# Kernel tuning notes

Hardware: AMD Instinct MI355X
Metric: run time of the kernel (lower is better)

## Reference

```python
import jax, jax.numpy as jnp
import numpy as np

DIM_Q = 512
DIM_K = 512
D_Q4 = float(DIM_Q) ** 0.25  # torch: dim_q ** (1/4)
D_K4 = float(DIM_K) ** 0.25


def setup_inputs() -> dict:
    key = jax.random.key(0)
    ks = jax.random.split(key, 9)
    B, N, D_IN = 8, 4096, 512
    s_in = 1.0 / np.sqrt(D_IN)
    return {
        "x_q": jax.random.normal(ks[0], (B, N, D_IN), jnp.float32),
        "x_k": jax.random.normal(ks[1], (B, N, D_IN), jnp.float32),
        "x_v": jax.random.normal(ks[2], (B, N, D_IN), jnp.float32),
        # Linear params stored as [in, out] for x @ W + b
        "W_q": jax.random.uniform(ks[3], (D_IN, DIM_Q), jnp.float32, -s_in, s_in),
        "b_q": jax.random.uniform(ks[4], (DIM_Q,), jnp.float32, -s_in, s_in),
        "W_k": jax.random.uniform(ks[5], (D_IN, DIM_K), jnp.float32, -s_in, s_in),
        "b_k": jax.random.uniform(ks[6], (DIM_K,), jnp.float32, -s_in, s_in),
        "W_v": jax.random.uniform(ks[7], (D_IN, DIM_K), jnp.float32, -s_in, s_in),
        "b_v": jax.random.uniform(ks[8], (DIM_K,), jnp.float32, -s_in, s_in),
    }


def reference(x_q, x_k, x_v, W_q, b_q, W_k, b_k, W_v, b_v):
    Q = x_q @ W_q + b_q          # [B, n, dq]
    K = x_k @ W_k + b_k          # [B, n, dk]
    V = x_v @ W_v + b_v          # [B, n, dk]
    # softmax_row: over sequence axis (dim=-2) of Q
    A = jax.nn.softmax(Q / D_Q4, axis=-2)          # [B, n, dq]
    # softmax_col on K^T (dim=-1) == softmax over sequence axis of K
    Ks = jax.nn.softmax(K / D_K4, axis=-2)         # [B, n, dk]
    Bm = jnp.einsum("bnd,bne->bde", Ks, V)        # [B, dk, dk]
    Z = jnp.einsum("bnd,bde->bne", A, Bm)         # [B, n, dk]
    return Z
```

## Files before the change

kernel.cpp:

```cpp
#include <hip/hip_runtime.h>
#include <hip/hip_bf16.h>


typedef __bf16 bf16_t;
typedef __attribute__((ext_vector_type(8))) __bf16 bf16x8;
typedef __attribute__((ext_vector_type(4))) float f32x4;

#define MFMA_BF16 __builtin_amdgcn_mfma_f32_16x16x32_bf16

__device__ inline void async_ld16(const void* g, void* l) {
  __builtin_amdgcn_global_load_lds(
      (const __attribute__((address_space(1))) void*)g,
      (__attribute__((address_space(3))) void*)l, 16, 0, 0);
}

#define INV_D4 0.2102241038134287f

__global__ __launch_bounds__(256) void wt_kernel(
    const float* __restrict__ Wq, const float* __restrict__ Wk,
    const float* __restrict__ Wv, bf16_t* __restrict__ Wt) {
  const int z = blockIdx.z;
  const float* W = (z == 0) ? Wq : (z == 1) ? Wk : Wv;
  bf16_t* O = Wt + (size_t)z * 262144;
  __shared__ __align__(16) bf16_t tile[64 * 72];
  const int t = threadIdx.x;
  const int r = t >> 2;
  const int c4 = (t & 3) * 16;
  const int in0 = blockIdx.x * 64, out0 = blockIdx.y * 64;
  const float* src = W + (size_t)(in0 + r) * 512 + out0 + c4;
#pragma unroll
  for (int i = 0; i < 4; ++i) {
    float4 f = ((const float4*)src)[i];
    tile[(c4 + i * 4 + 0) * 72 + r] = (__bf16)f.x;
    tile[(c4 + i * 4 + 1) * 72 + r] = (__bf16)f.y;
    tile[(c4 + i * 4 + 2) * 72 + r] = (__bf16)f.z;
    tile[(c4 + i * 4 + 3) * 72 + r] = (__bf16)f.w;
  }
  __syncthreads();
  bf16x8* dst = (bf16x8*)(O + (size_t)(out0 + r) * 512 + in0 + c4);
  const bf16x8* s = (const bf16x8*)(tile + r * 72 + c4);
  dst[0] = s[0];
  dst[1] = s[1];
}

__global__ __launch_bounds__(256, 2) void proj_kernel(
    const float* __restrict__ xq, const float* __restrict__ xk,
    const float* __restrict__ xv, const bf16_t* __restrict__ Wt,
    const float* __restrict__ bq, const float* __restrict__ bk,
    const float* __restrict__ bv, bf16_t* __restrict__ Eq,
    bf16_t* __restrict__ Ft, bf16_t* __restrict__ Vt,
    float* __restrict__ Sq, float* __restrict__ Sk) {
  const int z = blockIdx.z;
  const float* X = (z == 0) ? xq : (z == 1) ? xk : xv;
  const float* bias = (z == 0) ? bq : (z == 1) ? bk : bv;
  const bf16_t* W = Wt + (size_t)z * 262144;

  __shared__ __align__(16) union U {
    struct {
      bf16_t As[4096];
      bf16_t Bs[4096];
    } s;
    bf16_t T[128 * 136];
  } u;

  const int t = threadIdx.x;
  const int lane = t & 63, w = t >> 6;
  const int quad = lane >> 4, l15 = lane & 15;
  const int m0 = blockIdx.x * 128;
  const int n0 = blockIdx.y * 128;
  const int m_off = (w & 1) * 64, n_off = (w >> 1) * 64;

  f32x4 acc[4][4];
  const f32x4 zero4 = {0.f, 0.f, 0.f, 0.f};
#pragma unroll
  for (int i = 0; i < 4; ++i)
#pragma unroll
    for (int j = 0; j < 4; ++j) acc[i][j] = zero4;

  const int ar = t >> 1;
  const int ac = (t & 1) * 16;
  const float* abase = X + (size_t)(m0 + ar) * 512 + ac;

  float4 f0 = ((const float4*)abase)[0];
  float4 f1 = ((const float4*)abase)[1];
  float4 f2 = ((const float4*)abase)[2];
  float4 f3 = ((const float4*)abase)[3];

  for (int ks = 0; ks < 16; ++ks) {
    bf16x8 p0, p1;
    p0[0] = (__bf16)f0.x; p0[1] = (__bf16)f0.y; p0[2] = (__bf16)f0.z; p0[3] = (__bf16)f0.w;
    p0[4] = (__bf16)f1.x; p0[5] = (__bf16)f1.y; p0[6] = (__bf16)f1.z; p0[7] = (__bf16)f1.w;
    p1[0] = (__bf16)f2.x; p1[1] = (__bf16)f2.y; p1[2] = (__bf16)f2.z; p1[3] = (__bf16)f2.w;
    p1[4] = (__bf16)f3.x; p1[5] = (__bf16)f3.y; p1[6] = (__bf16)f3.z; p1[7] = (__bf16)f3.w;
    ((bf16x8*)u.s.As)[(ac >> 3) * 128 + ar] = p0;
    ((bf16x8*)u.s.As)[((ac >> 3) + 1) * 128 + ar] = p1;

#pragma unroll
    for (int i = 0; i < 2; ++i) {
      const int j = w * 2 + i;
      const int k8 = j >> 1;
      const int r = ((j & 1) << 6) + lane;
      async_ld16(W + (size_t)(n0 + r) * 512 + ks * 32 + k8 * 8, u.s.Bs + j * 512);
    }
    __syncthreads();

    bf16x8 af[4], bfr[4];
#pragma unroll
    for (int mi = 0; mi < 4; ++mi)
      af[mi] = ((const bf16x8*)u.s.As)[quad * 128 + m_off + mi * 16 + l15];
#pragma unroll
    for (int ni = 0; ni < 4; ++ni)
      bfr[ni] = ((const bf16x8*)u.s.Bs)[quad * 128 + n_off + ni * 16 + l15];

    if (ks < 15) {
      const float4* p = (const float4*)(abase + (ks + 1) * 32);
      f0 = p[0]; f1 = p[1]; f2 = p[2]; f3 = p[3];
    }

#pragma unroll
    for (int mi = 0; mi < 4; ++mi)
#pragma unroll
      for (int ni = 0; ni < 4; ++ni)
        acc[mi][ni] = MFMA_BF16(af[mi], bfr[ni], acc[mi][ni], 0, 0, 0);
    __syncthreads();
  }

  const int b = m0 >> 12;
  if (z == 0) {
    float cs[4] = {0.f, 0.f, 0.f, 0.f};
#pragma unroll
    for (int ni = 0; ni < 4; ++ni) {
      const int col = n0 + n_off + ni * 16 + l15;
      const float bv_ = bias[col];
#pragma unroll
      for (int mi = 0; mi < 4; ++mi)
#pragma unroll
        for (int r = 0; r < 4; ++r) {
          const int row = m0 + m_off + mi * 16 + quad * 4 + r;
          float v = __expf((acc[mi][ni][r] + bv_) * INV_D4);
          Eq[(size_t)row * 512 + col] = (bf16_t)v;
          cs[ni] += v;
        }
    }
#pragma unroll
    for (int ni = 0; ni < 4; ++ni) {
      cs[ni] += __shfl_xor(cs[ni], 16);
      cs[ni] += __shfl_xor(cs[ni], 32);
    }
    if (lane < 16) {
#pragma unroll
      for (int ni = 0; ni < 4; ++ni)
        atomicAdd(&Sq[b * 512 + n0 + n_off + ni * 16 + lane], cs[ni]);
    }
  } else {
    const bool expm = (z == 1);
    float cs[4] = {0.f, 0.f, 0.f, 0.f};
#pragma unroll
    for (int ni = 0; ni < 4; ++ni) {
      const int colc = n_off + ni * 16 + l15;
      const float bv_ = bias[n0 + colc];
#pragma unroll
      for (int mi = 0; mi < 4; ++mi)
#pragma unroll
        for (int r = 0; r < 4; ++r) {
          const int rowr = m_off + mi * 16 + quad * 4 + r;
          float v = acc[mi][ni][r] + bv_;
          if (expm) {
            v = __expf(v * INV_D4);
            cs[ni] += v;
          }
          u.T[colc * 136 + rowr] = (bf16_t)v;
        }
    }
    if (expm) {
#pragma unroll
      for (int ni = 0; ni < 4; ++ni) {
        cs[ni] += __shfl_xor(cs[ni], 16);
        cs[ni] += __shfl_xor(cs[ni], 32);
      }
      if (lane < 16) {
#pragma unroll
        for (int ni = 0; ni < 4; ++ni)
          atomicAdd(&Sk[b * 512 + n0 + n_off + ni * 16 + lane], cs[ni]);
      }
    }
    __syncthreads();
    bf16_t* Out = expm ? Ft : Vt;
    const int nloc = m0 & 4095;
    const int c = t >> 1;
    const int rh = (t & 1) * 64;
    bf16_t* dst = Out + (size_t)b * 2097152 + (size_t)(n0 + c) * 4096 + nloc + rh;
    const bf16_t* srcT = u.T + c * 136 + rh;
#pragma unroll
    for (int j = 0; j < 8; ++j) ((bf16x8*)dst)[j] = ((const bf16x8*)srcT)[j];
  }
}

__global__ __launch_bounds__(256, 2) void bm_gemm(
    const bf16_t* __restrict__ Ft, const bf16_t* __restrict__ Vt,
    float* __restrict__ Bmp) {
  const int b = blockIdx.z >> 1;
  const int s = blockIdx.z & 1;
  const int d0 = blockIdx.x * 128;
  const int e0 = blockIdx.y * 128;
  const bf16_t* A = Ft + (size_t)b * 2097152;
  const bf16_t* B = Vt + (size_t)b * 2097152;
  float* out = Bmp + ((size_t)s * 8 + b) * 262144;

  __shared__ __align__(16) bf16_t As[4096];
  __shared__ __align__(16) bf16_t Bs[4096];

  const int t = threadIdx.x;
  const int lane = t & 63, w = t >> 6;
  const int quad = lane >> 4, l15 = lane & 15;
  const int m_off = (w & 1) * 64, n_off = (w >> 1) * 64;

  f32x4 acc[4][4];
  const f32x4 zero4 = {0.f, 0.f, 0.f, 0.f};
#pragma unroll
  for (int i = 0; i < 4; ++i)
#pragma unroll
    for (int j = 0; j < 4; ++j) acc[i][j] = zero4;

  for (int ks = 0; ks < 64; ++ks) {
    const int k0 = s * 2048 + ks * 32;
#pragma unroll
    for (int i = 0; i < 2; ++i) {
      const int j = w * 2 + i;
      const int k8 = j >> 1;
      const int r = ((j & 1) << 6) + lane;
      async_ld16(A + (size_t)(d0 + r) * 4096 + k0 + k8 * 8, As + j * 512);
      async_ld16(B + (size_t)(e0 + r) * 4096 + k0 + k8 * 8, Bs + j * 512);
    }
    __syncthreads();
    bf16x8 af[4], bfr[4];
#pragma unroll
    for (int mi = 0; mi < 4; ++mi)
      af[mi] = ((const bf16x8*)As)[quad * 128 + m_off + mi * 16 + l15];
#pragma unroll
    for (int ni = 0; ni < 4; ++ni)
      bfr[ni] = ((const bf16x8*)Bs)[quad * 128 + n_off + ni * 16 + l15];
#pragma unroll
    for (int mi = 0; mi < 4; ++mi)
#pragma unroll
      for (int ni = 0; ni < 4; ++ni)
        acc[mi][ni] = MFMA_BF16(af[mi], bfr[ni], acc[mi][ni], 0, 0, 0);
    __syncthreads();
  }

#pragma unroll
  for (int mi = 0; mi < 4; ++mi)
#pragma unroll
    for (int ni = 0; ni < 4; ++ni) {
      const int ecol = e0 + n_off + ni * 16 + l15;
#pragma unroll
      for (int r = 0; r < 4; ++r) {
        const int drow = d0 + m_off + mi * 16 + quad * 4 + r;
        out[(size_t)drow * 512 + ecol] = acc[mi][ni][r];
      }
    }
}

__global__ __launch_bounds__(256) void scale_kernel(
    const float* __restrict__ Bmp, const float* __restrict__ Sq,
    const float* __restrict__ Sk, bf16_t* __restrict__ Ct) {
  const int b = blockIdx.z;
  const int d0 = blockIdx.x * 64, e0 = blockIdx.y * 64;
  __shared__ __align__(16) bf16_t tile[64 * 72];
  const int t = threadIdx.x;
  const int r = t >> 2;
  const int c4 = (t & 3) * 16;
  const int d = d0 + r;
  const float f = 1.0f / (Sq[b * 512 + d] * Sk[b * 512 + d]);
  const float* p0 = Bmp + (size_t)b * 262144 + (size_t)d * 512 + e0 + c4;
  const float* p1 = p0 + 2097152;
#pragma unroll
  for (int i = 0; i < 4; ++i) {
    float4 v0 = ((const float4*)p0)[i];
    float4 v1 = ((const float4*)p1)[i];
    tile[(c4 + i * 4 + 0) * 72 + r] = (__bf16)((v0.x + v1.x) * f);
    tile[(c4 + i * 4 + 1) * 72 + r] = (__bf16)((v0.y + v1.y) * f);
    tile[(c4 + i * 4 + 2) * 72 + r] = (__bf16)((v0.z + v1.z) * f);
    tile[(c4 + i * 4 + 3) * 72 + r] = (__bf16)((v0.w + v1.w) * f);
  }
  __syncthreads();
  bf16x8* dst = (bf16x8*)(Ct + (size_t)b * 262144 + (size_t)(e0 + r) * 512 + d0 + c4);
  const bf16x8* s = (const bf16x8*)(tile + r * 72 + c4);
  dst[0] = s[0];
  dst[1] = s[1];
}

__global__ __launch_bounds__(256, 2) void z_gemm(
    const bf16_t* __restrict__ Eq, const bf16_t* __restrict__ Ct,
    float* __restrict__ out) {
  __shared__ __align__(16) bf16_t As[4096];
  __shared__ __align__(16) bf16_t Bs[4096];

  const int t = threadIdx.x;
  const int lane = t & 63, w = t >> 6;
  const int quad = lane >> 4, l15 = lane & 15;
  const int m0 = blockIdx.x * 128;
  const int n0 = blockIdx.y * 128;
  const int batch = m0 >> 12;
  const bf16_t* Bt = Ct + (size_t)batch * 262144;
  const int m_off = (w & 1) * 64, n_off = (w >> 1) * 64;

  f32x4 acc[4][4];
  const f32x4 zero4 = {0.f, 0.f, 0.f, 0.f};
#pragma unroll
  for (int i = 0; i < 4; ++i)
#pragma unroll
    for (int j = 0; j < 4; ++j) acc[i][j] = zero4;

  for (int ks = 0; ks < 16; ++ks) {
    const int k0 = ks * 32;
#pragma unroll
    for (int i = 0; i < 2; ++i) {
      const int j = w * 2 + i;
      const int k8 = j >> 1;
      const int r = ((j & 1) << 6) + lane;
      async_ld16(Eq + (size_t)(m0 + r) * 512 + k0 + k8 * 8, As + j * 512);
      async_ld16(Bt + (size_t)(n0 + r) * 512 + k0 + k8 * 8, Bs + j * 512);
    }
    __syncthreads();
    bf16x8 af[4], bfr[4];
#pragma unroll
    for (int mi = 0; mi < 4; ++mi)
      af[mi] = ((const bf16x8*)As)[quad * 128 + m_off + mi * 16 + l15];
#pragma unroll
    for (int ni = 0; ni < 4; ++ni)
      bfr[ni] = ((const bf16x8*)Bs)[quad * 128 + n_off + ni * 16 + l15];
#pragma unroll
    for (int mi = 0; mi < 4; ++mi)
#pragma unroll
      for (int ni = 0; ni < 4; ++ni)
        acc[mi][ni] = MFMA_BF16(af[mi], bfr[ni], acc[mi][ni], 0, 0, 0);
    __syncthreads();
  }

#pragma unroll
  for (int mi = 0; mi < 4; ++mi)
#pragma unroll
    for (int ni = 0; ni < 4; ++ni) {
      const int col = n0 + n_off + ni * 16 + l15;
#pragma unroll
      for (int r = 0; r < 4; ++r) {
        const int row = m0 + m_off + mi * 16 + quad * 4 + r;
        out[(size_t)row * 512 + col] = acc[mi][ni][r];
      }
    }
}

extern "C" void kernel_launch(void* const* d_in, const int* in_sizes, int n_in,
                              void* d_out, int out_size, void* d_ws,
                              size_t ws_size, hipStream_t stream) {
  const float* xq = (const float*)d_in[0];
  const float* xk = (const float*)d_in[1];
  const float* xv = (const float*)d_in[2];
  const float* Wq = (const float*)d_in[3];
  const float* bq = (const float*)d_in[4];
  const float* Wk = (const float*)d_in[5];
  const float* bk = (const float*)d_in[6];
  const float* Wv = (const float*)d_in[7];
  const float* bv = (const float*)d_in[8];
  float* out = (float*)d_out;

  char* ws = (char*)d_ws;
  bf16_t* Eq = (bf16_t*)(ws + 0);
  bf16_t* Ft = (bf16_t*)(ws + 33554432);
  bf16_t* Vt = (bf16_t*)(ws + 67108864);
  bf16_t* Wt = (bf16_t*)(ws + 100663296);
  float* Sq = (float*)(ws + 102236160);
  float* Sk = (float*)(ws + 102252544);
  float* Bmp = (float*)(ws + 102268928);
  bf16_t* Ct = (bf16_t*)(ws + 33554432);

  hipMemsetAsync(ws + 102236160, 0, 32768, stream);

  wt_kernel<<<dim3(8, 8, 3), 256, 0, stream>>>(Wq, Wk, Wv, Wt);
  proj_kernel<<<dim3(256, 4, 3), 256, 0, stream>>>(xq, xk, xv, Wt, bq, bk, bv,
                                                   Eq, Ft, Vt, Sq, Sk);
  bm_gemm<<<dim3(4, 4, 16), 256, 0, stream>>>(Ft, Vt, Bmp);
  scale_kernel<<<dim3(8, 8, 8), 256, 0, stream>>>(Bmp, Sq, Sk, Ct);
  z_gemm<<<dim3(256, 4, 1), 256, 0, stream>>>(Eq, Ct, out);
}
```

Before: 439.3 us.

## Pre-convert inputs to bf16 and compute K/V projections transposed directly

Adds a separate fp32-to-bf16 conversion pass that stages the inputs in the output buffer, so the projection GEMM can load both operands with async global-to-LDS copies. For K and V the GEMM is swapped to produce the transposed result directly, removing the LDS transpose stage. The K column sums move into a separate reduction kernel instead of atomics. This adds extra global traffic (writing and re-reading the bf16 copies, plus the reduction pass), extra launches, and output stores that are only partly coalesced.

```diff
diff --git a/kernel.cpp b/kernel.cpp
--- a/kernel.cpp
+++ b/kernel.cpp
@@ -43,32 +43,43 @@
   dst[1] = s[1];
 }
 
+__global__ __launch_bounds__(256) void conv_kernel(
+    const float* __restrict__ a, const float* __restrict__ b,
+    bf16_t* __restrict__ oa, bf16_t* __restrict__ ob) {
+  const float* src = (blockIdx.z == 0) ? a : b;
+  bf16_t* dst = (blockIdx.z == 0) ? oa : ob;
+  const size_t i = ((size_t)blockIdx.x * 256 + threadIdx.x) * 8;
+  float4 f0 = ((const float4*)(src + i))[0];
+  float4 f1 = ((const float4*)(src + i))[1];
+  bf16x8 p;
+  p[0] = (__bf16)f0.x; p[1] = (__bf16)f0.y; p[2] = (__bf16)f0.z; p[3] = (__bf16)f0.w;
+  p[4] = (__bf16)f1.x; p[5] = (__bf16)f1.y; p[6] = (__bf16)f1.z; p[7] = (__bf16)f1.w;
+  *(bf16x8*)(dst + i) = p;
+}
+
 __global__ __launch_bounds__(256, 2) void proj_kernel(
-    const float* __restrict__ xq, const float* __restrict__ xk,
-    const float* __restrict__ xv, const bf16_t* __restrict__ Wt,
-    const float* __restrict__ bq, const float* __restrict__ bk,
-    const float* __restrict__ bv, bf16_t* __restrict__ Eq,
-    bf16_t* __restrict__ Ft, bf16_t* __restrict__ Vt,
-    float* __restrict__ Sq, float* __restrict__ Sk) {
-  const int z = blockIdx.z;
-  const float* X = (z == 0) ? xq : (z == 1) ? xk : xv;
-  const float* bias = (z == 0) ? bq : (z == 1) ? bk : bv;
+    const bf16_t* __restrict__ Xa, const bf16_t* __restrict__ Xb_,
+    const bf16_t* __restrict__ Wt, const float* __restrict__ biasa,
+    const float* __restrict__ biasb, bf16_t* __restrict__ Eq,
+    bf16_t* __restrict__ Fo, bf16_t* __restrict__ Vo, float* __restrict__ Sq,
+    int zoff) {
+  const int z = blockIdx.z + zoff;
+  const bf16_t* X = (z == 1) ? Xb_ : Xa;
+  const float* bias = (z == 1) ? biasb : biasa;
   const bf16_t* W = Wt + (size_t)z * 262144;
 
-  __shared__ __align__(16) union U {
-    struct {
-      bf16_t As[4096];
-      bf16_t Bs[4096];
-    } s;
-    bf16_t T[128 * 136];
-  } u;
+  __shared__ __align__(16) bf16_t As[4096];
+  __shared__ __align__(16) bf16_t Bs[4096];
 
   const int t = threadIdx.x;
   const int lane = t & 63, w = t >> 6;
   const int quad = lane >> 4, l15 = lane & 15;
   const int m0 = blockIdx.x * 128;
-  const int n0 = blockIdx.y * 128;
+  const int w0 = blockIdx.y * 128;
   const int m_off = (w & 1) * 64, n_off = (w >> 1) * 64;
+
+  const bf16_t* Abase = (z == 0) ? X + (size_t)m0 * 512 : W + (size_t)w0 * 512;
+  const bf16_t* Bbase = (z == 0) ? W + (size_t)w0 * 512 : X + (size_t)m0 * 512;
 
   f32x4 acc[4][4];
   const f32x4 zero4 = {0.f, 0.f, 0.f, 0.f};
@@ -77,46 +88,24 @@
 #pragma unroll
     for (int j = 0; j < 4; ++j) acc[i][j] = zero4;
 
-  const int ar = t >> 1;
-  const int ac = (t & 1) * 16;
-  const float* abase = X + (size_t)(m0 + ar) * 512 + ac;
-
-  float4 f0 = ((const float4*)abase)[0];
-  float4 f1 = ((const float4*)abase)[1];
-  float4 f2 = ((const float4*)abase)[2];
-  float4 f3 = ((const float4*)abase)[3];
-
   for (int ks = 0; ks < 16; ++ks) {
-    bf16x8 p0, p1;
-    p0[0] = (__bf16)f0.x; p0[1] = (__bf16)f0.y; p0[2] = (__bf16)f0.z; p0[3] = (__bf16)f0.w;
-    p0[4] = (__bf16)f1.x; p0[5] = (__bf16)f1.y; p0[6] = (__bf16)f1.z; p0[7] = (__bf16)f1.w;
-    p1[0] = (__bf16)f2.x; p1[1] = (__bf16)f2.y; p1[2] = (__bf16)f2.z; p1[3] = (__bf16)f2.w;
-    p1[4] = (__bf16)f3.x; p1[5] = (__bf16)f3.y; p1[6] = (__bf16)f3.z; p1[7] = (__bf16)f3.w;
-    ((bf16x8*)u.s.As)[(ac >> 3) * 128 + ar] = p0;
-    ((bf16x8*)u.s.As)[((ac >> 3) + 1) * 128 + ar] = p1;
-
+    const int k0 = ks * 32;
 #pragma unroll
     for (int i = 0; i < 2; ++i) {
       const int j = w * 2 + i;
       const int k8 = j >> 1;
       const int r = ((j & 1) << 6) + lane;
-      async_ld16(W + (size_t)(n0 + r) * 512 + ks * 32 + k8 * 8, u.s.Bs + j * 512);
-    }
-    __syncthreads();
-
+      async_ld16(Abase + (size_t)r * 512 + k0 + k8 * 8, As + j * 512);
+      async_ld16(Bbase + (size_t)r * 512 + k0 + k8 * 8, Bs + j * 512);
+    }
+    __syncthreads();
     bf16x8 af[4], bfr[4];
 #pragma unroll
     for (int mi = 0; mi < 4; ++mi)
-      af[mi] = ((const bf16x8*)u.s.As)[quad * 128 + m_off + mi * 16 + l15];
+      af[mi] = ((const bf16x8*)As)[quad * 128 + m_off + mi * 16 + l15];
 #pragma unroll
     for (int ni = 0; ni < 4; ++ni)
-      bfr[ni] = ((const bf16x8*)u.s.Bs)[quad * 128 + n_off + ni * 16 + l15];
-
-    if (ks < 15) {
-      const float4* p = (const float4*)(abase + (ks + 1) * 32);
-      f0 = p[0]; f1 = p[1]; f2 = p[2]; f3 = p[3];
-    }
-
+      bfr[ni] = ((const bf16x8*)Bs)[quad * 128 + n_off + ni * 16 + l15];
 #pragma unroll
     for (int mi = 0; mi < 4; ++mi)
 #pragma unroll
@@ -130,7 +119,7 @@
     float cs[4] = {0.f, 0.f, 0.f, 0.f};
 #pragma unroll
     for (int ni = 0; ni < 4; ++ni) {
-      const int col = n0 + n_off + ni * 16 + l15;
+      const int col = w0 + n_off + ni * 16 + l15;
       const float bv_ = bias[col];
 #pragma unroll
       for (int mi = 0; mi < 4; ++mi)
@@ -150,50 +139,44 @@
     if (lane < 16) {
 #pragma unroll
       for (int ni = 0; ni < 4; ++ni)
-        atomicAdd(&Sq[b * 512 + n0 + n_off + ni * 16 + lane], cs[ni]);
+        atomicAdd(&Sq[b * 512 + w0 + n_off + ni * 16 + lane], cs[ni]);
     }
   } else {
     const bool expm = (z == 1);
-    float cs[4] = {0.f, 0.f, 0.f, 0.f};
-#pragma unroll
-    for (int ni = 0; ni < 4; ++ni) {
-      const int colc = n_off + ni * 16 + l15;
-      const float bv_ = bias[n0 + colc];
-#pragma unroll
-      for (int mi = 0; mi < 4; ++mi)
-#pragma unroll
-        for (int r = 0; r < 4; ++r) {
-          const int rowr = m_off + mi * 16 + quad * 4 + r;
+    bf16_t* Out = expm ? Fo : Vo;
+    const int nl0 = (m0 & 4095) + n_off;
+#pragma unroll
+    for (int mi = 0; mi < 4; ++mi)
+#pragma unroll
+      for (int r = 0; r < 4; ++r) {
+        const int d = w0 + m_off + mi * 16 + quad * 4 + r;
+        const float bv_ = bias[d];
+        bf16_t* rowp = Out + (size_t)b * 2097152 + (size_t)d * 4096 + nl0;
+#pragma unroll
+        for (int ni = 0; ni < 4; ++ni) {
           float v = acc[mi][ni][r] + bv_;
-          if (expm) {
-            v = __expf(v * INV_D4);
-            cs[ni] += v;
-          }
-          u.T[colc * 136 + rowr] = (bf16_t)v;
+          if (expm) v = __expf(v * INV_D4);
+          rowp[ni * 16 + l15] = (bf16_t)v;
         }
-    }
-    if (expm) {
-#pragma unroll
-      for (int ni = 0; ni < 4; ++ni) {
-        cs[ni] += __shfl_xor(cs[ni], 16);
-        cs[ni] += __shfl_xor(cs[ni], 32);
       }
-      if (lane < 16) {
-#pragma unroll
-        for (int ni = 0; ni < 4; ++ni)
-          atomicAdd(&Sk[b * 512 + n0 + n_off + ni * 16 + lane], cs[ni]);
-      }
-    }
-    __syncthreads();
-    bf16_t* Out = expm ? Ft : Vt;
-    const int nloc = m0 & 4095;
-    const int c = t >> 1;
-    const int rh = (t & 1) * 64;
-    bf16_t* dst = Out + (size_t)b * 2097152 + (size_t)(n0 + c) * 4096 + nloc + rh;
-    const bf16_t* srcT = u.T + c * 136 + rh;
-#pragma unroll
-    for (int j = 0; j < 8; ++j) ((bf16x8*)dst)[j] = ((const bf16x8*)srcT)[j];
-  }
+  }
+}
+
+__global__ __launch_bounds__(256) void sk_kernel(const bf16_t* __restrict__ Ft,
+                                                 float* __restrict__ Sk) {
+  const int row = blockIdx.x * 4 + (threadIdx.x >> 6);
+  const int lane = threadIdx.x & 63;
+  const bf16x8* p = (const bf16x8*)(Ft + (size_t)row * 4096) + lane;
+  float s = 0.f;
+#pragma unroll
+  for (int j = 0; j < 8; ++j) {
+    bf16x8 v = p[j * 64];
+#pragma unroll
+    for (int e = 0; e < 8; ++e) s += (float)v[e];
+  }
+#pragma unroll
+  for (int m = 1; m <= 32; m <<= 1) s += __shfl_xor(s, m);
+  if (lane == 0) Sk[row] = s;
 }
 
 __global__ __launch_bounds__(256, 2) void bm_gemm(
@@ -369,17 +352,26 @@
   bf16_t* Eq = (bf16_t*)(ws + 0);
   bf16_t* Ft = (bf16_t*)(ws + 33554432);
   bf16_t* Vt = (bf16_t*)(ws + 67108864);
-  bf16_t* Wt = (bf16_t*)(ws + 100663296);
-  float* Sq = (float*)(ws + 102236160);
-  float* Sk = (float*)(ws + 102252544);
-  float* Bmp = (float*)(ws + 102268928);
+  float* Bmp = (float*)(ws + 100663296);
+  bf16_t* Wt = (bf16_t*)(ws + 117440512);
+  float* Sq = (float*)(ws + 119013376);
+  float* Sk = (float*)(ws + 119029760);
   bf16_t* Ct = (bf16_t*)(ws + 33554432);
 
-  hipMemsetAsync(ws + 102236160, 0, 32768, stream);
+  bf16_t* Xqb = (bf16_t*)d_out;
+  bf16_t* Xkb = (bf16_t*)((char*)d_out + 33554432);
+  bf16_t* Xvb = (bf16_t*)d_out;
+
+  hipMemsetAsync(Sq, 0, 16384, stream);
 
   wt_kernel<<<dim3(8, 8, 3), 256, 0, stream>>>(Wq, Wk, Wv, Wt);
-  proj_kernel<<<dim3(256, 4, 3), 256, 0, stream>>>(xq, xk, xv, Wt, bq, bk, bv,
-                                                   Eq, Ft, Vt, Sq, Sk);
+  conv_kernel<<<dim3(8192, 1, 2), 256, 0, stream>>>(xq, xk, Xqb, Xkb);
+  proj_kernel<<<dim3(256, 4, 2), 256, 0, stream>>>(Xqb, Xkb, Wt, bq, bk, Eq, Ft,
+                                                   Vt, Sq, 0);
+  conv_kernel<<<dim3(8192, 1, 1), 256, 0, stream>>>(xv, xv, Xvb, Xvb);
+  proj_kernel<<<dim3(256, 4, 1), 256, 0, stream>>>(Xvb, Xvb, Wt, bv, bv, Eq, Ft,
+                                                   Vt, Sq, 2);
+  sk_kernel<<<dim3(1024), 256, 0, stream>>>(Ft, Sk);
   bm_gemm<<<dim3(4, 4, 16), 256, 0, stream>>>(Ft, Vt, Bmp);
   scale_kernel<<<dim3(8, 8, 8), 256, 0, stream>>>(Bmp, Sq, Sk, Ct);
   z_gemm<<<dim3(256, 4, 1), 256, 0, stream>>>(Eq, Ct, out);
```

Measured after the change: 456.1 us. +3.8%, slower.
